# Optimization experiments

Measured on AMD Instinct MI355X. Metric: run time of the kernel, lower is better.

Reference implementation:

```python
import jax, jax.numpy as jnp
import numpy as np

N, L, H, D = 2, 2048, 8, 64
DIM = H * D  # 512
P = 1  # position_dimension


def setup_inputs() -> dict:
    key = jax.random.key(0)
    ks = jax.random.split(key, 7)
    y = jax.random.normal(ks[0], (N, L, DIM), dtype=jnp.float32)
    # token positions, shape (N, L, P)
    positions = jnp.broadcast_to(
        jnp.arange(L, dtype=jnp.float32)[None, :, None], (N, L, P))
    scale = 0.02
    Wq = jax.random.normal(ks[1], (DIM, DIM), dtype=jnp.float32) * scale
    Wk = jax.random.normal(ks[2], (DIM, DIM), dtype=jnp.float32) * scale
    Wv = jax.random.normal(ks[3], (DIM, DIM), dtype=jnp.float32) * scale
    position_coeffs = jnp.ones((H, D), dtype=jnp.float32)
    # small so cos(pq - pk) stays near 1 and scaled scores are well-conditioned
    position_weight = jax.random.normal(ks[4], (H, D, P), dtype=jnp.float32) * 0.01
    position_bias = jax.random.normal(ks[5], (H, D), dtype=jnp.float32) * 0.01
    return {"y": y, "positions": positions, "Wq": Wq, "Wk": Wk, "Wv": Wv,
            "position_coeffs": position_coeffs,
            "position_weight": position_weight,
            "position_bias": position_bias}


def reference(y, positions, Wq, Wk, Wv, position_coeffs, position_weight,
              position_bias):
    n, l, _ = y.shape
    # QKV projections; kernel_function (softplus, i.e. log(1+exp)) on q and k
    q = jax.nn.softplus(y @ Wq.T).reshape(n, l, H, D).transpose(0, 2, 1, 3)
    k = jax.nn.softplus(y @ Wk.T).reshape(n, l, H, D).transpose(0, 2, 1, 3)
    v = (y @ Wv.T).reshape(n, l, H, D).transpose(0, 2, 1, 3)
    # projected positions pq = pk : (N, H, L, D)
    p = jnp.einsum('hdp,nlp->nhld', position_weight, positions) \
        + position_bias[None, :, None, :]
    cos_p, sin_p = jnp.cos(p), jnp.sin(p)
    # score_ij = sum_d q_d k_d c_d (cos pq_d cos pk_d + sin pq_d sin pk_d)
    coeff = position_coeffs[None, :, None, :]
    qc, kc = q * coeff * cos_p, k * cos_p
    qs, ks = q * coeff * sin_p, k * sin_p
    score = jnp.einsum('nhqd,nhkd->nhqk', qc, kc) \
          + jnp.einsum('nhqd,nhkd->nhqk', qs, ks)
    # mask_future (future_offset = 0): zero out keys j > i
    causal = jnp.tril(jnp.ones((l, l), dtype=bool))
    score = jnp.where(causal[None, None], score, 0.0)
    # scaled: scores sum to 1 along keys
    score = score / jnp.sum(score, axis=-1, keepdims=True)
    att = jnp.einsum('nhqk,nhkd->nhqd', score, v)
    return att.transpose(0, 2, 1, 3).reshape(n, l, DIM)
```

## Files before the change

kernel.cpp:

```cpp
#include <hip/hip_runtime.h>
#include <hip/hip_bf16.h>

typedef __attribute__((ext_vector_type(8))) short bf16x8;
typedef __attribute__((ext_vector_type(4))) float f32x4;
typedef unsigned int u32;

#define L_SEQ 2048
#define NHEAD 8
#define DHEAD 64
#define DMODEL 512
#define QK_STRIDE 262144
#define V_STRIDE  131072

__device__ __forceinline__ short f2bf(float f) {
    union { float f; unsigned u; } x; x.f = f;
    unsigned r = x.u + 0x7FFFu + ((x.u >> 16) & 1u);
    return (short)(r >> 16);
}

__device__ __forceinline__ void split1(float x, short& hi, short& lo) {
    unsigned uh = __float_as_uint(x) & 0xFFFF0000u;
    hi = (short)(uh >> 16);
    lo = f2bf(x - __uint_as_float(uh));
}

__device__ __forceinline__ void split8(const float* p, bf16x8& hi, bf16x8& lo) {
    #pragma unroll
    for (int i = 0; i < 8; ++i) {
        float x = p[i];
        unsigned uh = __float_as_uint(x) & 0xFFFF0000u;
        hi[i] = (short)(uh >> 16);
        lo[i] = f2bf(x - __uint_as_float(uh));
    }
}

__device__ __forceinline__ u32 cvtpk_bf16(float a, float b) {
    u32 r;
    asm("v_cvt_pk_bf16_f32 %0, %1, %2" : "=v"(r) : "v"(a), "v"(b));
    return r;
}

__device__ __forceinline__ void gload_lds16(const void* g, void* l) {
    __builtin_amdgcn_global_load_lds(
        (const __attribute__((address_space(1))) unsigned int*)g,
        (__attribute__((address_space(3))) unsigned int*)l, 16, 0, 0);
}

__global__ __launch_bounds__(256) void split_kernel(
    const float* __restrict__ y,
    const float* __restrict__ Wq, const float* __restrict__ Wk, const float* __restrict__ Wv,
    short* __restrict__ yh, short* __restrict__ yl,
    short* __restrict__ wh, short* __restrict__ wl)
{
    const int wv = threadIdx.x >> 6, ln = threadIdx.x & 63;
    const int u = blockIdx.x * 4 + wv;
    float tmp[8];
    if (u < 4096) {
        const int B = u >> 4, kb = u & 15;
        const int row = B*16 + (ln & 15);
        const int k   = kb*32 + (ln >> 4)*8;
        const float* src = y + (size_t)row * DMODEL + k;
        *(float4*)tmp       = *(const float4*)src;
        *(float4*)(tmp + 4) = *(const float4*)(src + 4);
        bf16x8 hi, lo;
        split8(tmp, hi, lo);
        const size_t dst = (size_t)u*512 + ln*8;
        *(bf16x8*)(yh + dst) = hi;
        *(bf16x8*)(yl + dst) = lo;
    } else {
        const int u2 = u - 4096;
        const int mat = u2 >> 9;
        const int r   = u2 & 511;
        const int C = r >> 4, kb = r & 15;
        const float* W = (mat == 0) ? Wq : (mat == 1) ? Wk : Wv;
        const int col = C*16 + (ln & 15);
        const int k   = kb*32 + (ln >> 4)*8;
        const float* src = W + (size_t)col * DMODEL + k;
        *(float4*)tmp       = *(const float4*)src;
        *(float4*)(tmp + 4) = *(const float4*)(src + 4);
        bf16x8 hi, lo;
        split8(tmp, hi, lo);
        const size_t dst = (size_t)u2*512 + ln*8;
        *(bf16x8*)(wh + dst) = hi;
        *(bf16x8*)(wl + dst) = lo;
    }
}

__global__ __launch_bounds__(256) void prep_kernel(
    const short* __restrict__ yh, const short* __restrict__ yl,
    const short* __restrict__ wh, const short* __restrict__ wl,
    const float* __restrict__ positions,
    const float* __restrict__ coeff, const float* __restrict__ pw, const float* __restrict__ pb,
    short* __restrict__ Qh, short* __restrict__ Ql,
    short* __restrict__ Kh, short* __restrict__ Kl,
    short* __restrict__ Vh, short* __restrict__ Vl)
{
    __shared__ float vtile[128][65];
    const int mode = blockIdx.z;
    const int m_base = blockIdx.x * 128;
    const int h = blockIdx.y;
    const int n_base = h * 64;
    const int tid = threadIdx.x;
    const int lane = tid & 63;
    const int wv = tid >> 6;
    const int lr = lane & 15;
    const int lg = lane >> 4;

    const short* whm = wh + (size_t)mode * 262144;
    const short* wlm = wl + (size_t)mode * 262144;
    const int Ba0 = blockIdx.x*8 + wv*2;

    f32x4 acc[2][4];
    #pragma unroll
    for (int t = 0; t < 2; ++t)
        #pragma unroll
        for (int c = 0; c < 4; ++c) acc[t][c] = (f32x4){0.f, 0.f, 0.f, 0.f};

    #pragma unroll 4
    for (int kb = 0; kb < 16; ++kb) {
        bf16x8 ah[2], al[2], bh[4], bl[4];
        #pragma unroll
        for (int t = 0; t < 2; ++t) {
            const size_t off = ((size_t)((Ba0 + t)*16 + kb)*64 + lane)*8;
            ah[t] = *(const bf16x8*)(yh + off);
            al[t] = *(const bf16x8*)(yl + off);
        }
        #pragma unroll
        for (int c = 0; c < 4; ++c) {
            const size_t off = ((size_t)((h*4 + c)*16 + kb)*64 + lane)*8;
            bh[c] = *(const bf16x8*)(whm + off);
            bl[c] = *(const bf16x8*)(wlm + off);
        }
        #pragma unroll
        for (int t = 0; t < 2; ++t)
            #pragma unroll
            for (int c = 0; c < 4; ++c) {
                acc[t][c] = __builtin_amdgcn_mfma_f32_16x16x32_bf16(ah[t], bh[c], acc[t][c], 0, 0, 0);
                acc[t][c] = __builtin_amdgcn_mfma_f32_16x16x32_bf16(ah[t], bl[c], acc[t][c], 0, 0, 0);
                acc[t][c] = __builtin_amdgcn_mfma_f32_16x16x32_bf16(al[t], bh[c], acc[t][c], 0, 0, 0);
            }
    }

    const int n_idx = m_base >> 11;
    const int nh = n_idx * NHEAD + h;

    if (mode == 2) {
        #pragma unroll
        for (int t = 0; t < 2; ++t)
            #pragma unroll
            for (int c = 0; c < 4; ++c)
                #pragma unroll
                for (int r = 0; r < 4; ++r)
                    vtile[wv*32 + t*16 + lg*4 + r][c*16 + lr] = acc[t][c][r];
        __syncthreads();
        const size_t vbase = (size_t)nh * V_STRIDE;
        #pragma unroll
        for (int i = 0; i < 32; ++i) {
            const int key_l = (tid & 7) + 8*(i & 15);
            const int d     = (tid >> 3) + 32*(i >> 4);
            const int key   = (m_base & (L_SEQ - 1)) + key_l;
            short th, tl;
            split1(vtile[key_l][d], th, tl);
            const size_t idx = vbase +
                ((size_t)((key >> 5)*4 + (d >> 4))*64 + (d & 15) + 16*((key >> 3) & 3))*8 + (key & 7);
            Vh[idx] = th; Vl[idx] = tl;
        }
    } else {
        short* OUTh = (mode == 0) ? Qh : Kh;
        short* OUTl = (mode == 0) ? Ql : Kl;
        const size_t qbase_nh = (size_t)nh * QK_STRIDE;
        #pragma unroll
        for (int t = 0; t < 2; ++t) {
            #pragma unroll
            for (int c = 0; c < 4; ++c) {
                const int d = c*16 + lr;
                const float pwv = pw[n_base + d];
                const float pbv = pb[n_base + d];
                const float cf  = (mode == 0) ? coeff[n_base + d] : 1.0f;
                const int lane_t = 16*((2*c + (lr >> 3)) & 3);
                const int j = lr & 7;
                #pragma unroll
                for (int r = 0; r < 4; ++r) {
                    const int gm = m_base + wv*32 + t*16 + lg*4 + r;
                    const int l = gm & (L_SEQ - 1);
                    const int B = l >> 4;
                    const float posv = positions[gm];
                    const float x = acc[t][c][r];
                    const float sp = fmaxf(x, 0.f) + __logf(1.f + __expf(-fabsf(x)));
                    const float p = pwv * posv + pbv;
                    const float cs = __cosf(p), sn = __sinf(p);
                    short h1, l1, h2, l2;
                    split1(sp * cf * cs, h1, l1);
                    split1(sp * cf * sn, h2, l2);
                    const int ln = (l & 15) + lane_t;
                    const size_t idx_c = qbase_nh + ((size_t)(B*4 + (c >> 1))*64 + ln)*8 + j;
                    const size_t idx_s = qbase_nh + ((size_t)(B*4 + 2 + (c >> 1))*64 + ln)*8 + j;
                    OUTh[idx_c] = h1; OUTl[idx_c] = l1;
                    OUTh[idx_s] = h2; OUTl[idx_s] = l2;
                }
            }
        }
    }
}

template<int CHUNK>
__global__ __launch_bounds__(256) void attn_kernel(
    const short* __restrict__ Qh, const short* __restrict__ Ql,
    const short* __restrict__ Kh, const short* __restrict__ Kl,
    const short* __restrict__ Vh, const short* __restrict__ Vl,
    float* __restrict__ O_part, float* __restrict__ rs_part)
{
    __shared__ char s_lds[65536];
    const int id = blockIdx.x;
    const int nh   = (id & 7)*2 + ((id >> 3) & 1);
    const int slot = id >> 4;

    int rem = slot, qt = 0;
    for (qt = 0; qt < 16; ++qt) {
        const int nch = (2*qt + 2 + CHUNK - 1) / CHUNK;
        if (rem < nch) break;
        rem -= nch;
    }
    const int nst = 2*qt + 2;
    const int kt0 = rem * CHUNK;
    const int kt1 = (kt0 + CHUNK < nst) ? (kt0 + CHUNK) : nst;

    const int q_base = qt * 128;
    const int tid = threadIdx.x;
    const int lane = tid & 63;
    const int wv = tid >> 6;
    const int lr = lane & 15;
    const int lg = lane >> 4;

    const short* Qh_b = Qh + (size_t)nh * QK_STRIDE;
    const short* Ql_b = Ql + (size_t)nh * QK_STRIDE;
    const short* Kh_b = Kh + (size_t)nh * QK_STRIDE;
    const short* Kl_b = Kl + (size_t)nh * QK_STRIDE;
    const short* Vh_b = Vh + (size_t)nh * V_STRIDE;
    const short* Vl_b = Vl + (size_t)nh * V_STRIDE;

    bf16x8 qh[2][4], ql[2][4];
    #pragma unroll
    for (int t = 0; t < 2; ++t) {
        const int Bq = qt*8 + wv*2 + t;
        #pragma unroll
        for (int kh = 0; kh < 4; ++kh) {
            const size_t off = ((size_t)(Bq*4 + kh)*64 + lane)*8;
            qh[t][kh] = *(const bf16x8*)(Qh_b + off);
            ql[t][kh] = *(const bf16x8*)(Ql_b + off);
        }
    }

    f32x4 o_acc[2][4];
    float rs[2];
    #pragma unroll
    for (int t = 0; t < 2; ++t) {
        #pragma unroll
        for (int c = 0; c < 4; ++c) o_acc[t][c] = (f32x4){0.f, 0.f, 0.f, 0.f};
        rs[t] = 0.f;
    }

    const int addr0 = (lr + ((lg & 1) * 2) * 16) << 2;
    const int addr1 = addr0 + 64;
    const bool selhi = (lg >= 2);
    const int lb = lane << 4;

    {
        const char* kh_src = (const char*)(Kh_b + (size_t)kt0*8192);
        const char* kl_src = (const char*)(Kl_b + (size_t)kt0*8192);
        #pragma unroll
        for (int i = 0; i < 8; ++i) {
            const int ch = wv*8 + i;
            const char* src = (ch < 16) ? kh_src + ch*1024 : kl_src + (ch-16)*1024;
            gload_lds16(src + lb, s_lds + ch*1024);
        }
    }
    __syncthreads();

    int cur = 0;
    for (int kt = kt0; kt < kt1; ++kt) {
        if (kt + 1 < kt1) {
            const char* kh_src = (const char*)(Kh_b + (size_t)(kt+1)*8192);
            const char* kl_src = (const char*)(Kl_b + (size_t)(kt+1)*8192);
            char* dst = s_lds + (cur ? 0 : 32768);
            #pragma unroll
            for (int i = 0; i < 8; ++i) {
                const int ch = wv*8 + i;
                const char* src = (ch < 16) ? kh_src + ch*1024 : kl_src + (ch-16)*1024;
                gload_lds16(src + lb, dst + ch*1024);
            }
        }

        bf16x8 vfh[2][4], vfl[2][4];
        #pragma unroll
        for (int kc = 0; kc < 2; ++kc)
            #pragma unroll
            for (int cd = 0; cd < 4; ++cd) {
                const size_t voff = ((size_t)((kt*2 + kc)*4 + cd)*64 + lane)*8;
                vfh[kc][cd] = *(const bf16x8*)(Vh_b + voff);
                vfl[kc][cd] = *(const bf16x8*)(Vl_b + voff);
            }

        const char* kbuf = s_lds + (cur ? 32768 : 0);
        f32x4 st[2][4];
        #pragma unroll
        for (int t = 0; t < 2; ++t)
            #pragma unroll
            for (int c = 0; c < 4; ++c) st[t][c] = (f32x4){0.f, 0.f, 0.f, 0.f};

        #pragma unroll
        for (int c = 0; c < 4; ++c) {
            #pragma unroll
            for (int kh = 0; kh < 4; ++kh) {
                const int boff = (c*4 + kh)*1024 + lb;
                const bf16x8 kfh = *(const bf16x8*)(kbuf + boff);
                const bf16x8 kfl = *(const bf16x8*)(kbuf + 16384 + boff);
                #pragma unroll
                for (int t = 0; t < 2; ++t) {
                    st[t][c] = __builtin_amdgcn_mfma_f32_16x16x32_bf16(kfh, qh[t][kh], st[t][c], 0, 0, 0);
                    st[t][c] = __builtin_amdgcn_mfma_f32_16x16x32_bf16(kfh, ql[t][kh], st[t][c], 0, 0, 0);
                    st[t][c] = __builtin_amdgcn_mfma_f32_16x16x32_bf16(kfl, qh[t][kh], st[t][c], 0, 0, 0);
                }
            }
        }

        const int k0 = kt * 64;
        const bool domask = (kt >= 2*qt);
        #pragma unroll
        for (int t = 0; t < 2; ++t) {
            const int gq = q_base + wv*32 + t*16 + lr;
            float part = 0.f;
            #pragma unroll
            for (int c = 0; c < 4; ++c)
                #pragma unroll
                for (int r = 0; r < 4; ++r) {
                    const int gk = k0 + c*16 + lg*4 + r;
                    float v = st[t][c][r];
                    if (domask && gk > gq) v = 0.f;
                    st[t][c][r] = v;
                    part += v;
                }
            part += __shfl_xor(part, 16);
            part += __shfl_xor(part, 32);
            rs[t] += part;
        }

        u32 pwh[2][4][2], pwl[2][4][2];
        #pragma unroll
        for (int t = 0; t < 2; ++t)
            #pragma unroll
            for (int c = 0; c < 4; ++c) {
                const u32 b0 = __float_as_uint(st[t][c][0]);
                const u32 b1 = __float_as_uint(st[t][c][1]);
                const u32 b2 = __float_as_uint(st[t][c][2]);
                const u32 b3 = __float_as_uint(st[t][c][3]);
                pwh[t][c][0] = (b1 & 0xFFFF0000u) | (b0 >> 16);
                pwh[t][c][1] = (b3 & 0xFFFF0000u) | (b2 >> 16);
                const float l0 = st[t][c][0] - __uint_as_float(b0 & 0xFFFF0000u);
                const float l1 = st[t][c][1] - __uint_as_float(b1 & 0xFFFF0000u);
                const float l2 = st[t][c][2] - __uint_as_float(b2 & 0xFFFF0000u);
                const float l3 = st[t][c][3] - __uint_as_float(b3 & 0xFFFF0000u);
                pwl[t][c][0] = cvtpk_bf16(l0, l1);
                pwl[t][c][1] = cvtpk_bf16(l2, l3);
            }

        #pragma unroll
        for (int kc = 0; kc < 2; ++kc) {
            union { u32 u[4]; bf16x8 v; } pah[2], pal[2];
            #pragma unroll
            for (int t = 0; t < 2; ++t) {
                u32 a, b;
                a = (u32)__builtin_amdgcn_ds_bpermute(addr0, (int)pwh[t][2*kc][0]);
                b = (u32)__builtin_amdgcn_ds_bpermute(addr0, (int)pwh[t][2*kc+1][0]);
                pah[t].u[0] = selhi ? b : a;
                a = (u32)__builtin_amdgcn_ds_bpermute(addr0, (int)pwh[t][2*kc][1]);
                b = (u32)__builtin_amdgcn_ds_bpermute(addr0, (int)pwh[t][2*kc+1][1]);
                pah[t].u[1] = selhi ? b : a;
                a = (u32)__builtin_amdgcn_ds_bpermute(addr1, (int)pwh[t][2*kc][0]);
                b = (u32)__builtin_amdgcn_ds_bpermute(addr1, (int)pwh[t][2*kc+1][0]);
                pah[t].u[2] = selhi ? b : a;
                a = (u32)__builtin_amdgcn_ds_bpermute(addr1, (int)pwh[t][2*kc][1]);
                b = (u32)__builtin_amdgcn_ds_bpermute(addr1, (int)pwh[t][2*kc+1][1]);
                pah[t].u[3] = selhi ? b : a;

                a = (u32)__builtin_amdgcn_ds_bpermute(addr0, (int)pwl[t][2*kc][0]);
                b = (u32)__builtin_amdgcn_ds_bpermute(addr0, (int)pwl[t][2*kc+1][0]);
                pal[t].u[0] = selhi ? b : a;
                a = (u32)__builtin_amdgcn_ds_bpermute(addr0, (int)pwl[t][2*kc][1]);
                b = (u32)__builtin_amdgcn_ds_bpermute(addr0, (int)pwl[t][2*kc+1][1]);
                pal[t].u[1] = selhi ? b : a;
                a = (u32)__builtin_amdgcn_ds_bpermute(addr1, (int)pwl[t][2*kc][0]);
                b = (u32)__builtin_amdgcn_ds_bpermute(addr1, (int)pwl[t][2*kc+1][0]);
                pal[t].u[2] = selhi ? b : a;
                a = (u32)__builtin_amdgcn_ds_bpermute(addr1, (int)pwl[t][2*kc][1]);
                b = (u32)__builtin_amdgcn_ds_bpermute(addr1, (int)pwl[t][2*kc+1][1]);
                pal[t].u[3] = selhi ? b : a;
            }
            #pragma unroll
            for (int cd = 0; cd < 4; ++cd) {
                #pragma unroll
                for (int t = 0; t < 2; ++t) {
                    o_acc[t][cd] = __builtin_amdgcn_mfma_f32_16x16x32_bf16(pah[t].v, vfh[kc][cd], o_acc[t][cd], 0, 0, 0);
                    o_acc[t][cd] = __builtin_amdgcn_mfma_f32_16x16x32_bf16(pah[t].v, vfl[kc][cd], o_acc[t][cd], 0, 0, 0);
                    o_acc[t][cd] = __builtin_amdgcn_mfma_f32_16x16x32_bf16(pal[t].v, vfh[kc][cd], o_acc[t][cd], 0, 0, 0);
                }
            }
        }
        __syncthreads();
        cur ^= 1;
    }

    const size_t slab = (size_t)slot * 16 + nh;
    #pragma unroll
    for (int t = 0; t < 2; ++t)
        if (lg == 0)
            rs_part[slab*128 + wv*32 + t*16 + lr] = rs[t];

    #pragma unroll
    for (int t = 0; t < 2; ++t)
        #pragma unroll
        for (int cd = 0; cd < 4; ++cd)
            #pragma unroll
            for (int r = 0; r < 4; ++r) {
                const int row = wv*32 + t*16 + lg*4 + r;
                O_part[slab*8192 + row*64 + cd*16 + lr] = o_acc[t][cd][r];
            }
}

template<int CHUNK>
__global__ __launch_bounds__(256) void reduce_div_kernel(
    const float* __restrict__ O_part, const float* __restrict__ rs_part,
    float* __restrict__ out)
{
    const int idx = blockIdx.x * 256 + threadIdx.x;
    const int d4 = idx & 15;
    const int l  = (idx >> 4) & (L_SEQ - 1);
    const int nh = idx >> 15;
    const int qt = l >> 7;
    const int row = l & 127;
    int cs = 0;
    for (int q = 0; q < qt; ++q) cs += (2*q + 2 + CHUNK - 1) / CHUNK;
    const int nch = (2*qt + 2 + CHUNK - 1) / CHUNK;

    float4 o = {0.f, 0.f, 0.f, 0.f};
    float rssum = 0.f;
    for (int ci = 0; ci < nch; ++ci) {
        const size_t slab = (size_t)(cs + ci) * 16 + nh;
        const float4 p = *(const float4*)(O_part + slab*8192 + row*64 + d4*4);
        o.x += p.x; o.y += p.y; o.z += p.z; o.w += p.w;
        rssum += rs_part[slab*128 + row];
    }
    const float inv = 1.0f / rssum;
    float4 r;
    r.x = o.x * inv; r.y = o.y * inv; r.z = o.z * inv; r.w = o.w * inv;
    const int n = nh >> 3, h = nh & 7;
    *(float4*)(out + ((size_t)(n*L_SEQ + l))*DMODEL + h*DHEAD + d4*4) = r;
}

extern "C" void kernel_launch(void* const* d_in, const int* in_sizes, int n_in,
                              void* d_out, int out_size, void* d_ws, size_t ws_size,
                              hipStream_t stream) {
    const float* y         = (const float*)d_in[0];
    const float* positions = (const float*)d_in[1];
    const float* Wq        = (const float*)d_in[2];
    const float* Wk        = (const float*)d_in[3];
    const float* Wv        = (const float*)d_in[4];
    const float* coeff     = (const float*)d_in[5];
    const float* pw        = (const float*)d_in[6];
    const float* pb        = (const float*)d_in[7];
    float* out = (float*)d_out;

    const size_t SQK = (size_t)16 * QK_STRIDE;
    const size_t SV  = (size_t)16 * V_STRIDE;
    const size_t SY  = (size_t)4096 * 512;
    const size_t SW  = (size_t)3 * 512 * 512;
    short* Qh = (short*)d_ws;
    short* Ql = Qh + SQK;
    short* Kh = Ql + SQK;
    short* Kl = Kh + SQK;
    short* Vh = Kl + SQK;
    short* Vl = Vh + SV;
    short* yh = Vl + SV;
    short* yl = yh + SY;
    short* wh = yl + SY;
    short* wl = wh + SW;
    float* O_part = (float*)(wl + SW);
    const size_t base_bytes = (SQK*4 + SV*2 + SY*2 + SW*2) * sizeof(short);
    const size_t per_slot   = (size_t)16 * (8192 + 128) * sizeof(float);

    split_kernel<<<dim3(1408), dim3(256), 0, stream>>>(y, Wq, Wk, Wv, yh, yl, wh, wl);
    prep_kernel<<<dim3(32, 8, 3), dim3(256), 0, stream>>>(
        yh, yl, wh, wl, positions, coeff, pw, pb, Qh, Ql, Kh, Kl, Vh, Vl);

    if (ws_size >= base_bytes + 72 * per_slot) {
        float* rs_part = O_part + (size_t)72 * 16 * 8192;
        attn_kernel<4><<<dim3(72 * 16), dim3(256), 0, stream>>>(
            Qh, Ql, Kh, Kl, Vh, Vl, O_part, rs_part);
        reduce_div_kernel<4><<<dim3(2048), dim3(256), 0, stream>>>(O_part, rs_part, out);
    } else {
        float* rs_part = O_part + (size_t)40 * 16 * 8192;
        attn_kernel<8><<<dim3(40 * 16), dim3(256), 0, stream>>>(
            Qh, Ql, Kh, Kl, Vh, Vl, O_part, rs_part);
        reduce_div_kernel<8><<<dim3(2048), dim3(256), 0, stream>>>(O_part, rs_part, out);
    }
}
```

Before: 101.5 us.

## Split attention block into eight waves each owning one 16-row query tile

The attention kernel now launches 512 threads (8 waves) per block instead of 256, and each wave handles one 16-row query tile instead of two. K tile staging into LDS is split across eight waves, four chunks each. This halves per-wave register use for Q fragments, accumulators and scores, and gives more waves per CU to hide latency. In exchange, each wave now reads the K fragments from LDS and the V fragments from global memory for only one query tile, which doubles those loads per unit of work, and more waves take part in each barrier.

```diff
diff --git a/kernel.cpp b/kernel.cpp
--- a/kernel.cpp
+++ b/kernel.cpp
@@ -204,7 +204,7 @@
 }
 
 template<int CHUNK>
-__global__ __launch_bounds__(256) void attn_kernel(
+__global__ __launch_bounds__(512) void attn_kernel(
     const short* __restrict__ Qh, const short* __restrict__ Ql,
     const short* __restrict__ Kh, const short* __restrict__ Kl,
     const short* __restrict__ Vh, const short* __restrict__ Vl,
@@ -239,26 +239,21 @@
     const short* Vh_b = Vh + (size_t)nh * V_STRIDE;
     const short* Vl_b = Vl + (size_t)nh * V_STRIDE;
 
-    bf16x8 qh[2][4], ql[2][4];
-    #pragma unroll
-    for (int t = 0; t < 2; ++t) {
-        const int Bq = qt*8 + wv*2 + t;
+    bf16x8 qh[4], ql[4];
+    {
+        const int Bq = qt*8 + wv;
         #pragma unroll
         for (int kh = 0; kh < 4; ++kh) {
             const size_t off = ((size_t)(Bq*4 + kh)*64 + lane)*8;
-            qh[t][kh] = *(const bf16x8*)(Qh_b + off);
-            ql[t][kh] = *(const bf16x8*)(Ql_b + off);
-        }
-    }
-
-    f32x4 o_acc[2][4];
-    float rs[2];
+            qh[kh] = *(const bf16x8*)(Qh_b + off);
+            ql[kh] = *(const bf16x8*)(Ql_b + off);
+        }
+    }
+
+    f32x4 o_acc[4];
+    float rs = 0.f;
     #pragma unroll
-    for (int t = 0; t < 2; ++t) {
-        #pragma unroll
-        for (int c = 0; c < 4; ++c) o_acc[t][c] = (f32x4){0.f, 0.f, 0.f, 0.f};
-        rs[t] = 0.f;
-    }
+    for (int c = 0; c < 4; ++c) o_acc[c] = (f32x4){0.f, 0.f, 0.f, 0.f};
 
     const int addr0 = (lr + ((lg & 1) * 2) * 16) << 2;
     const int addr1 = addr0 + 64;
@@ -269,8 +264,8 @@
         const char* kh_src = (const char*)(Kh_b + (size_t)kt0*8192);
         const char* kl_src = (const char*)(Kl_b + (size_t)kt0*8192);
         #pragma unroll
-        for (int i = 0; i < 8; ++i) {
-            const int ch = wv*8 + i;
+        for (int i = 0; i < 4; ++i) {
+            const int ch = wv*4 + i;
             const char* src = (ch < 16) ? kh_src + ch*1024 : kl_src + (ch-16)*1024;
             gload_lds16(src + lb, s_lds + ch*1024);
         }
@@ -284,8 +279,8 @@
             const char* kl_src = (const char*)(Kl_b + (size_t)(kt+1)*8192);
             char* dst = s_lds + (cur ? 0 : 32768);
             #pragma unroll
-            for (int i = 0; i < 8; ++i) {
-                const int ch = wv*8 + i;
+            for (int i = 0; i < 4; ++i) {
+                const int ch = wv*4 + i;
                 const char* src = (ch < 16) ? kh_src + ch*1024 : kl_src + (ch-16)*1024;
                 gload_lds16(src + lb, dst + ch*1024);
             }
@@ -302,11 +297,9 @@
             }
 
         const char* kbuf = s_lds + (cur ? 32768 : 0);
-        f32x4 st[2][4];
-        #pragma unroll
-        for (int t = 0; t < 2; ++t)
-            #pragma unroll
-            for (int c = 0; c < 4; ++c) st[t][c] = (f32x4){0.f, 0.f, 0.f, 0.f};
+        f32x4 st[4];
+        #pragma unroll
+        for (int c = 0; c < 4; ++c) st[c] = (f32x4){0.f, 0.f, 0.f, 0.f};
 
         #pragma unroll
         for (int c = 0; c < 4; ++c) {
@@ -315,95 +308,84 @@
                 const int boff = (c*4 + kh)*1024 + lb;
                 const bf16x8 kfh = *(const bf16x8*)(kbuf + boff);
                 const bf16x8 kfl = *(const bf16x8*)(kbuf + 16384 + boff);
-                #pragma unroll
-                for (int t = 0; t < 2; ++t) {
-                    st[t][c] = __builtin_amdgcn_mfma_f32_16x16x32_bf16(kfh, qh[t][kh], st[t][c], 0, 0, 0);
-                    st[t][c] = __builtin_amdgcn_mfma_f32_16x16x32_bf16(kfh, ql[t][kh], st[t][c], 0, 0, 0);
-                    st[t][c] = __builtin_amdgcn_mfma_f32_16x16x32_bf16(kfl, qh[t][kh], st[t][c], 0, 0, 0);
-                }
+                st[c] = __builtin_amdgcn_mfma_f32_16x16x32_bf16(kfh, qh[kh], st[c], 0, 0, 0);
+                st[c] = __builtin_amdgcn_mfma_f32_16x16x32_bf16(kfh, ql[kh], st[c], 0, 0, 0);
+                st[c] = __builtin_amdgcn_mfma_f32_16x16x32_bf16(kfl, qh[kh], st[c], 0, 0, 0);
             }
         }
 
         const int k0 = kt * 64;
         const bool domask = (kt >= 2*qt);
-        #pragma unroll
-        for (int t = 0; t < 2; ++t) {
-            const int gq = q_base + wv*32 + t*16 + lr;
+        {
+            const int gq = q_base + wv*16 + lr;
             float part = 0.f;
             #pragma unroll
             for (int c = 0; c < 4; ++c)
                 #pragma unroll
                 for (int r = 0; r < 4; ++r) {
                     const int gk = k0 + c*16 + lg*4 + r;
-                    float v = st[t][c][r];
+                    float v = st[c][r];
                     if (domask && gk > gq) v = 0.f;
-                    st[t][c][r] = v;
+                    st[c][r] = v;
                     part += v;
                 }
             part += __shfl_xor(part, 16);
             part += __shfl_xor(part, 32);
-            rs[t] += part;
-        }
-
-        u32 pwh[2][4][2], pwl[2][4][2];
-        #pragma unroll
-        for (int t = 0; t < 2; ++t)
-            #pragma unroll
-            for (int c = 0; c < 4; ++c) {
-                const u32 b0 = __float_as_uint(st[t][c][0]);
-                const u32 b1 = __float_as_uint(st[t][c][1]);
-                const u32 b2 = __float_as_uint(st[t][c][2]);
-                const u32 b3 = __float_as_uint(st[t][c][3]);
-                pwh[t][c][0] = (b1 & 0xFFFF0000u) | (b0 >> 16);
-                pwh[t][c][1] = (b3 & 0xFFFF0000u) | (b2 >> 16);
-                const float l0 = st[t][c][0] - __uint_as_float(b0 & 0xFFFF0000u);
-                const float l1 = st[t][c][1] - __uint_as_float(b1 & 0xFFFF0000u);
-                const float l2 = st[t][c][2] - __uint_as_float(b2 & 0xFFFF0000u);
-                const float l3 = st[t][c][3] - __uint_as_float(b3 & 0xFFFF0000u);
-                pwl[t][c][0] = cvtpk_bf16(l0, l1);
-                pwl[t][c][1] = cvtpk_bf16(l2, l3);
-            }
+            rs += part;
+        }
+
+        u32 pwh[4][2], pwl[4][2];
+        #pragma unroll
+        for (int c = 0; c < 4; ++c) {
+            const u32 b0 = __float_as_uint(st[c][0]);
+            const u32 b1 = __float_as_uint(st[c][1]);
+            const u32 b2 = __float_as_uint(st[c][2]);
+            const u32 b3 = __float_as_uint(st[c][3]);
+            pwh[c][0] = (b1 & 0xFFFF0000u) | (b0 >> 16);
+            pwh[c][1] = (b3 & 0xFFFF0000u) | (b2 >> 16);
+            const float l0 = st[c][0] - __uint_as_float(b0 & 0xFFFF0000u);
+            const float l1 = st[c][1] - __uint_as_float(b1 & 0xFFFF0000u);
+            const float l2 = st[c][2] - __uint_as_float(b2 & 0xFFFF0000u);
+            const float l3 = st[c][3] - __uint_as_float(b3 & 0xFFFF0000u);
+            pwl[c][0] = cvtpk_bf16(l0, l1);
+            pwl[c][1] = cvtpk_bf16(l2, l3);
+        }
 
         #pragma unroll
         for (int kc = 0; kc < 2; ++kc) {
-            union { u32 u[4]; bf16x8 v; } pah[2], pal[2];
-            #pragma unroll
-            for (int t = 0; t < 2; ++t) {
-                u32 a, b;
-                a = (u32)__builtin_amdgcn_ds_bpermute(addr0, (int)pwh[t][2*kc][0]);
-                b = (u32)__builtin_amdgcn_ds_bpermute(addr0, (int)pwh[t][2*kc+1][0]);
-                pah[t].u[0] = selhi ? b : a;
-                a = (u32)__builtin_amdgcn_ds_bpermute(addr0, (int)pwh[t][2*kc][1]);
-                b = (u32)__builtin_amdgcn_ds_bpermute(addr0, (int)pwh[t][2*kc+1][1]);
-                pah[t].u[1] = selhi ? b : a;
-                a = (u32)__builtin_amdgcn_ds_bpermute(addr1, (int)pwh[t][2*kc][0]);
-                b = (u32)__builtin_amdgcn_ds_bpermute(addr1, (int)pwh[t][2*kc+1][0]);
-                pah[t].u[2] = selhi ? b : a;
-                a = (u32)__builtin_amdgcn_ds_bpermute(addr1, (int)pwh[t][2*kc][1]);
-                b = (u32)__builtin_amdgcn_ds_bpermute(addr1, (int)pwh[t][2*kc+1][1]);
-                pah[t].u[3] = selhi ? b : a;
-
-                a = (u32)__builtin_amdgcn_ds_bpermute(addr0, (int)pwl[t][2*kc][0]);
-                b = (u32)__builtin_amdgcn_ds_bpermute(addr0, (int)pwl[t][2*kc+1][0]);
-                pal[t].u[0] = selhi ? b : a;
-                a = (u32)__builtin_amdgcn_ds_bpermute(addr0, (int)pwl[t][2*kc][1]);
-                b = (u32)__builtin_amdgcn_ds_bpermute(addr0, (int)pwl[t][2*kc+1][1]);
-                pal[t].u[1] = selhi ? b : a;
-                a = (u32)__builtin_amdgcn_ds_bpermute(addr1, (int)pwl[t][2*kc][0]);
-                b = (u32)__builtin_amdgcn_ds_bpermute(addr1, (int)pwl[t][2*kc+1][0]);
-                pal[t].u[2] = selhi ? b : a;
-                a = (u32)__builtin_amdgcn_ds_bpermute(addr1, (int)pwl[t][2*kc][1]);
-                b = (u32)__builtin_amdgcn_ds_bpermute(addr1, (int)pwl[t][2*kc+1][1]);
-                pal[t].u[3] = selhi ? b : a;
-            }
+            union { u32 u[4]; bf16x8 v; } pah, pal;
+            u32 a, b;
+            a = (u32)__builtin_amdgcn_ds_bpermute(addr0, (int)pwh[2*kc][0]);
+            b = (u32)__builtin_amdgcn_ds_bpermute(addr0, (int)pwh[2*kc+1][0]);
+            pah.u[0] = selhi ? b : a;
+            a = (u32)__builtin_amdgcn_ds_bpermute(addr0, (int)pwh[2*kc][1]);
+            b = (u32)__builtin_amdgcn_ds_bpermute(addr0, (int)pwh[2*kc+1][1]);
+            pah.u[1] = selhi ? b : a;
+            a = (u32)__builtin_amdgcn_ds_bpermute(addr1, (int)pwh[2*kc][0]);
+            b = (u32)__builtin_amdgcn_ds_bpermute(addr1, (int)pwh[2*kc+1][0]);
+            pah.u[2] = selhi ? b : a;
+            a = (u32)__builtin_amdgcn_ds_bpermute(addr1, (int)pwh[2*kc][1]);
+            b = (u32)__builtin_amdgcn_ds_bpermute(addr1, (int)pwh[2*kc+1][1]);
+            pah.u[3] = selhi ? b : a;
+
+            a = (u32)__builtin_amdgcn_ds_bpermute(addr0, (int)pwl[2*kc][0]);
+            b = (u32)__builtin_amdgcn_ds_bpermute(addr0, (int)pwl[2*kc+1][0]);
+            pal.u[0] = selhi ? b : a;
+            a = (u32)__builtin_amdgcn_ds_bpermute(addr0, (int)pwl[2*kc][1]);
+            b = (u32)__builtin_amdgcn_ds_bpermute(addr0, (int)pwl[2*kc+1][1]);
+            pal.u[1] = selhi ? b : a;
+            a = (u32)__builtin_amdgcn_ds_bpermute(addr1, (int)pwl[2*kc][0]);
+            b = (u32)__builtin_amdgcn_ds_bpermute(addr1, (int)pwl[2*kc+1][0]);
+            pal.u[2] = selhi ? b : a;
+            a = (u32)__builtin_amdgcn_ds_bpermute(addr1, (int)pwl[2*kc][1]);
+            b = (u32)__builtin_amdgcn_ds_bpermute(addr1, (int)pwl[2*kc+1][1]);
+            pal.u[3] = selhi ? b : a;
+
             #pragma unroll
             for (int cd = 0; cd < 4; ++cd) {
-                #pragma unroll
-                for (int t = 0; t < 2; ++t) {
-                    o_acc[t][cd] = __builtin_amdgcn_mfma_f32_16x16x32_bf16(pah[t].v, vfh[kc][cd], o_acc[t][cd], 0, 0, 0);
-                    o_acc[t][cd] = __builtin_amdgcn_mfma_f32_16x16x32_bf16(pah[t].v, vfl[kc][cd], o_acc[t][cd], 0, 0, 0);
-                    o_acc[t][cd] = __builtin_amdgcn_mfma_f32_16x16x32_bf16(pal[t].v, vfh[kc][cd], o_acc[t][cd], 0, 0, 0);
-                }
+                o_acc[cd] = __builtin_amdgcn_mfma_f32_16x16x32_bf16(pah.v, vfh[kc][cd], o_acc[cd], 0, 0, 0);
+                o_acc[cd] = __builtin_amdgcn_mfma_f32_16x16x32_bf16(pah.v, vfl[kc][cd], o_acc[cd], 0, 0, 0);
+                o_acc[cd] = __builtin_amdgcn_mfma_f32_16x16x32_bf16(pal.v, vfh[kc][cd], o_acc[cd], 0, 0, 0);
             }
         }
         __syncthreads();
@@ -411,20 +393,16 @@
     }
 
     const size_t slab = (size_t)slot * 16 + nh;
+    if (lg == 0)
+        rs_part[slab*128 + wv*16 + lr] = rs;
+
     #pragma unroll
-    for (int t = 0; t < 2; ++t)
-        if (lg == 0)
-            rs_part[slab*128 + wv*32 + t*16 + lr] = rs[t];
-
-    #pragma unroll
-    for (int t = 0; t < 2; ++t)
-        #pragma unroll
-        for (int cd = 0; cd < 4; ++cd)
-            #pragma unroll
-            for (int r = 0; r < 4; ++r) {
-                const int row = wv*32 + t*16 + lg*4 + r;
-                O_part[slab*8192 + row*64 + cd*16 + lr] = o_acc[t][cd][r];
-            }
+    for (int cd = 0; cd < 4; ++cd)
+        #pragma unroll
+        for (int r = 0; r < 4; ++r) {
+            const int row = wv*16 + lg*4 + r;
+            O_part[slab*8192 + row*64 + cd*16 + lr] = o_acc[cd][r];
+        }
 }
 
 template<int CHUNK>
@@ -494,12 +472,12 @@
 
     if (ws_size >= base_bytes + 72 * per_slot) {
         float* rs_part = O_part + (size_t)72 * 16 * 8192;
-        attn_kernel<4><<<dim3(72 * 16), dim3(256), 0, stream>>>(
+        attn_kernel<4><<<dim3(72 * 16), dim3(512), 0, stream>>>(
             Qh, Ql, Kh, Kl, Vh, Vl, O_part, rs_part);
         reduce_div_kernel<4><<<dim3(2048), dim3(256), 0, stream>>>(O_part, rs_part, out);
     } else {
         float* rs_part = O_part + (size_t)40 * 16 * 8192;
-        attn_kernel<8><<<dim3(40 * 16), dim3(256), 0, stream>>>(
+        attn_kernel<8><<<dim3(40 * 16), dim3(512), 0, stream>>>(
             Qh, Ql, Kh, Kl, Vh, Vl, O_part, rs_part);
         reduce_div_kernel<8><<<dim3(2048), dim3(256), 0, stream>>>(O_part, rs_part, out);
     }
```

Result: faster. 95.62 us (median of 2 runs) (-5.8%).
